# Optimization experiments

Measured on AMD Instinct MI355X. Metric: run time of the kernel, lower is better.

Reference implementation:

```python
import jax, jax.numpy as jnp
import numpy as np
import math

B, T, D = 8, 1024, 1024
N, L = 256, 768
H = 16
TE = 2048  # time_embed_dim
EPS = 1e-5


def _ln(x, g, b):
    mu = jnp.mean(x, axis=-1, keepdims=True)
    var = jnp.mean(jnp.square(x - mu), axis=-1, keepdims=True)
    return (x - mu) * jax.lax.rsqrt(var + EPS) * g + b


def setup_inputs() -> dict:
    key = jax.random.key(0)
    ks = jax.random.split(key, 16)
    s = lambda fan_in: 1.0 / math.sqrt(fan_in)
    return {
        "x": jax.random.normal(ks[0], (B, T, D), jnp.float32),
        "xf": jax.random.normal(ks[1], (B, N, L), jnp.float32),
        "emb": jax.random.normal(ks[2], (B, TE), jnp.float32),
        "ln_g": jnp.ones((D,), jnp.float32),
        "ln_b": jnp.zeros((D,), jnp.float32),
        "cln_g": jnp.ones((L,), jnp.float32),
        "cln_b": jnp.zeros((L,), jnp.float32),
        "Wq": jax.random.normal(ks[3], (D, D), jnp.float32) * s(D),
        "bq": jnp.zeros((D,), jnp.float32),
        "Wk": jax.random.normal(ks[4], (L, D), jnp.float32) * s(L),
        "bk": jnp.zeros((D,), jnp.float32),
        "Wv": jax.random.normal(ks[5], (L, D), jnp.float32) * s(L),
        "bv": jnp.zeros((D,), jnp.float32),
        "sln_g": jnp.ones((D,), jnp.float32),
        "sln_b": jnp.zeros((D,), jnp.float32),
        "Wemb": jax.random.normal(ks[6], (TE, 2 * D), jnp.float32) * s(TE),
        "bemb": jnp.zeros((2 * D,), jnp.float32),
        "Wout": jax.random.normal(ks[7], (D, D), jnp.float32) * s(D) * 0.02,
        "bout": jnp.zeros((D,), jnp.float32),
    }


def reference(x, xf, emb, ln_g, ln_b, cln_g, cln_b, Wq, bq, Wk, bk, Wv, bv,
              sln_g, sln_b, Wemb, bemb, Wout, bout):
    # x: (B,T,D), xf: (B,N,L), emb: (B,TE)
    hd = D // H
    q = (_ln(x, ln_g, ln_b) @ Wq + bq).reshape(B, T, H, hd)
    xf_n = _ln(xf, cln_g, cln_b)
    k = (xf_n @ Wk + bk).reshape(B, N, H, hd)
    v = (xf_n @ Wv + bv).reshape(B, N, H, hd)
    # scores: (B,T,N,H); note: scaled by sqrt(D//H)
    att = jnp.einsum('bthd,bnhd->btnh', q, k) / math.sqrt(hd)
    w = jax.nn.softmax(att, axis=2)  # softmax over conditioning tokens N
    y = jnp.einsum('btnh,bnhd->bthd', w, v).reshape(B, T, D)
    # StylizationBlock (dropout = 0)
    emb_out = jax.nn.silu(emb) @ Wemb + bemb  # (B, 2D)
    scale, shift = jnp.split(emb_out[:, None, :], 2, axis=2)
    h = _ln(y, sln_g, sln_b) * (1.0 + scale) + shift
    h = jax.nn.silu(h) @ Wout + bout
    return x + h
```

## Files before the change

kernel.cpp:

```cpp
#include <hip/hip_runtime.h>
#include <hip/hip_bf16.h>

typedef __hip_bfloat16 bf16;
typedef unsigned short ushort;
typedef __attribute__((ext_vector_type(8))) short bf16x8;
typedef __attribute__((ext_vector_type(4))) float f32x4;

#define B_ 8
#define T_ 1024
#define D_ 1024
#define N_ 256
#define L_ 768
#define H_ 16
#define HD_ 64
#define TE_ 2048

__device__ __forceinline__ void gld16(const void* g, void* l) {
    __builtin_amdgcn_global_load_lds((const __attribute__((address_space(1))) void*)g,
                                     (__attribute__((address_space(3))) void*)l,
                                     16, 0, 0);
}

__device__ __forceinline__ float bitf(unsigned u) { return __uint_as_float(u); }

__global__ __launch_bounds__(256) void prep_kernel(
        const float* __restrict__ x, const float* __restrict__ xf,
        const float* __restrict__ g1, const float* __restrict__ b1,
        const float* __restrict__ g2, const float* __restrict__ b2,
        const float* __restrict__ Wq, const float* __restrict__ Wk,
        const float* __restrict__ Wv, const float* __restrict__ Wo,
        const float* __restrict__ emb, const float* __restrict__ Wemb,
        bf16* __restrict__ out1, bf16* __restrict__ out2,
        bf16* __restrict__ wqt, bf16* __restrict__ wkt,
        bf16* __restrict__ wvt, bf16* __restrict__ wot,
        float* __restrict__ part) {
    __shared__ __align__(16) char smem[16384];
    int bid = blockIdx.x;
    int tid = threadIdx.x;
    if (bid < 10240) {
        const float *rp, *g, *bb; bf16* op; int cols;
        if (bid < B_ * T_) {
            rp = x + (size_t)bid * D_; g = g1; bb = b1; op = out1 + (size_t)bid * D_; cols = D_;
        } else {
            int r = bid - B_ * T_;
            rp = xf + (size_t)r * L_; g = g2; bb = b2; op = out2 + (size_t)r * L_; cols = L_;
        }
        float* ps  = (float*)smem;
        float* ps2 = ps + 4;
        float* st  = ps + 8;
        bool act = tid * 4 < cols;
        float4 v = act ? *(const float4*)&rp[tid * 4] : make_float4(0.f, 0.f, 0.f, 0.f);
        float s = v.x + v.y + v.z + v.w;
        float s2 = v.x * v.x + v.y * v.y + v.z * v.z + v.w * v.w;
        for (int off = 32; off; off >>= 1) {
            s  += __shfl_down(s,  off, 64);
            s2 += __shfl_down(s2, off, 64);
        }
        int wid = tid >> 6, lid = tid & 63;
        if (lid == 0) { ps[wid] = s; ps2[wid] = s2; }
        __syncthreads();
        if (tid == 0) {
            float t = ps[0] + ps[1] + ps[2] + ps[3];
            float t2 = ps2[0] + ps2[1] + ps2[2] + ps2[3];
            float m = t / cols;
            float var = t2 / cols - m * m;
            st[0] = m; st[1] = rsqrtf(var + 1e-5f);
        }
        __syncthreads();
        if (!act) return;
        float mu = st[0], rstd = st[1];
        float4 gv = *(const float4*)&g[tid * 4];
        float4 bv = *(const float4*)&bb[tid * 4];
        float o0 = (v.x - mu) * rstd * gv.x + bv.x;
        float o1 = (v.y - mu) * rstd * gv.y + bv.y;
        float o2 = (v.z - mu) * rstd * gv.z + bv.z;
        float o3 = (v.w - mu) * rstd * gv.w + bv.w;
        ushort4 uo;
        bf16 h0 = __float2bfloat16(o0); uo.x = *(ushort*)&h0;
        bf16 h1 = __float2bfloat16(o1); uo.y = *(ushort*)&h1;
        bf16 h2 = __float2bfloat16(o2); uo.z = *(ushort*)&h2;
        bf16 h3 = __float2bfloat16(o3); uo.w = *(ushort*)&h3;
        *(ushort4*)&op[tid * 4] = uo;
    } else if (bid < 11136) {
        ushort (*t)[65] = (ushort(*)[65])smem;
        int id = bid - 10240;
        int xb = id & 15, y = id >> 4;
        const float* W; bf16* Wt; int K, ky;
        if (y < 16)      { W = Wq; Wt = wqt; K = 1024; ky = y; }
        else if (y < 28) { W = Wk; Wt = wkt; K = 768;  ky = y - 16; }
        else if (y < 40) { W = Wv; Wt = wvt; K = 768;  ky = y - 28; }
        else             { W = Wo; Wt = wot; K = 1024; ky = y - 40; }
        int k0 = ky * 64, n0 = xb * 64;
#pragma unroll
        for (int i = 0; i < 16; i++) {
            int e = tid + i * 256;
            int r = e >> 6, c = e & 63;
            bf16 hv = __float2bfloat16(W[(size_t)(k0 + r) * D_ + n0 + c]);
            t[r][c] = *(ushort*)&hv;
        }
        __syncthreads();
#pragma unroll
        for (int i = 0; i < 16; i++) {
            int e = tid + i * 256;
            int r = e >> 6, c = e & 63;
            ushort uv = t[c][r];
            Wt[(size_t)(n0 + r) * K + k0 + c] = *(bf16*)&uv;
        }
    } else {
        float* se  = (float*)smem;
        float* red = (float*)(smem + 8192);
        int id = bid - 11136;
        int j0 = (id & 31) * 64;
        int ks = id >> 5;
        int tx = tid & 15, ty = tid >> 4;
        int w = tid >> 6, lane = tid & 63;
#pragma unroll
        for (int b = 0; b < 8; b++) {
            float xv = emb[b * TE_ + ks * 256 + tid];
            se[b * 256 + tid] = xv / (1.f + __expf(-xv));
        }
        __syncthreads();
        float acc[8][4] = {};
#pragma unroll 4
        for (int i = 0; i < 16; i++) {
            int e = ty + 16 * i;
            float4 wv = *(const float4*)&Wemb[(size_t)(ks * 256 + e) * 2048 + j0 + tx * 4];
#pragma unroll
            for (int b = 0; b < 8; b++) {
                float s = se[b * 256 + e];
                acc[b][0] += s * wv.x; acc[b][1] += s * wv.y;
                acc[b][2] += s * wv.z; acc[b][3] += s * wv.w;
            }
        }
#pragma unroll
        for (int b = 0; b < 8; b++)
#pragma unroll
            for (int m = 0; m < 4; m++) {
                float v = acc[b][m];
                v += __shfl_down(v, 32, 64);
                v += __shfl_down(v, 16, 64);
                if (lane < 16) red[(w * 8 + b) * 64 + lane * 4 + m] = v;
            }
        __syncthreads();
        for (int o = tid; o < 512; o += 256) {
            int b = o >> 6, jl = o & 63;
            float s = red[(0 * 8 + b) * 64 + jl] + red[(1 * 8 + b) * 64 + jl]
                    + red[(2 * 8 + b) * 64 + jl] + red[(3 * 8 + b) * 64 + jl];
            part[((size_t)ks * 8 + b) * 2048 + j0 + jl] = s;
        }
    }
}

template <int MODE>
__device__ __forceinline__ void gemm_body(const ushort* __restrict__ Ap,
                                          const ushort* __restrict__ Bp,
                                          const float* __restrict__ bias,
                                          const float* __restrict__ res,
                                          void* __restrict__ Cout,
                                          int m0, int n0, int Ncols, int K,
                                          ushort* Ash, ushort* Bsh) {
    int tid = threadIdx.x;
    int w = tid >> 6, lane = tid & 63;
    int quad = lane >> 4, l15 = lane & 15;
    int wm = (w >> 1) * 64, wn = (w & 1) * 32;
    int lr8 = lane >> 3;
    int sc  = lane & 7;
    int gc  = sc ^ lr8;
    f32x4 acc[4][2] = {};
    for (int kt = 0; kt < K; kt += 64) {
#pragma unroll
        for (int j = 0; j < 4; j++) {
            int rbase = w * 32 + j * 8;
            gld16(&Ap[(size_t)(m0 + rbase + lr8) * K + kt + gc * 8], &Ash[rbase * 64]);
        }
#pragma unroll
        for (int j = 0; j < 2; j++) {
            int rbase = w * 16 + j * 8;
            gld16(&Bp[(size_t)(n0 + rbase + lr8) * K + kt + gc * 8], &Bsh[rbase * 64]);
        }
        __syncthreads();
#pragma unroll
        for (int kh = 0; kh < 2; kh++) {
            bf16x8 af[4], bfr[2];
#pragma unroll
            for (int mt = 0; mt < 4; mt++)
                af[mt] = *(bf16x8*)&Ash[(wm + mt * 16 + l15) * 64 + (((kh * 4 + quad) ^ (l15 & 7)) * 8)];
#pragma unroll
            for (int nt = 0; nt < 2; nt++)
                bfr[nt] = *(bf16x8*)&Bsh[(wn + nt * 16 + l15) * 64 + (((kh * 4 + quad) ^ (l15 & 7)) * 8)];
#pragma unroll
            for (int mt = 0; mt < 4; mt++)
#pragma unroll
                for (int nt = 0; nt < 2; nt++)
                    acc[mt][nt] = __builtin_amdgcn_mfma_f32_16x16x32_bf16(af[mt], bfr[nt], acc[mt][nt], 0, 0, 0);
        }
        __syncthreads();
    }
#pragma unroll
    for (int mt = 0; mt < 4; mt++) {
#pragma unroll
        for (int nt = 0; nt < 2; nt++) {
#pragma unroll
            for (int reg = 0; reg < 4; reg++) {
                int row = m0 + wm + mt * 16 + quad * 4 + reg;
                int col = n0 + wn + nt * 16 + l15;
                float v = acc[mt][nt][reg] + bias[col];
                if (MODE == 1) {
                    v += res[(size_t)row * Ncols + col];
                    ((float*)Cout)[(size_t)row * Ncols + col] = v;
                } else if (MODE == 0) {
                    ((bf16*)Cout)[(size_t)row * Ncols + col] = __float2bfloat16(v);
                } else {
                    int b = row >> 8, n = row & 255;
                    int h = col >> 6, d = col & 63;
                    size_t addr = ((size_t)(b * 16 + h) * 64 + d) * 256
                                + (((n >> 3) ^ (d & 7)) * 8) + (n & 7);
                    ((bf16*)Cout)[addr] = __float2bfloat16(v);
                }
            }
        }
    }
}

__global__ __launch_bounds__(256) void qkv_gemm(const bf16* __restrict__ xn,
                                                const bf16* __restrict__ xfn,
                                                const bf16* __restrict__ wqt,
                                                const bf16* __restrict__ wkt,
                                                const bf16* __restrict__ wvt,
                                                const float* __restrict__ bq,
                                                const float* __restrict__ bk,
                                                const float* __restrict__ bv,
                                                bf16* __restrict__ q,
                                                bf16* __restrict__ kbuf,
                                                bf16* __restrict__ vT,
                                                const float* __restrict__ part,
                                                const float* __restrict__ bemb,
                                                float* __restrict__ embo) {
    __shared__ ushort Ash[128 * 64];
    __shared__ ushort Bsh[64 * 64];
    int bid = blockIdx.x;
    if (bid < 1024) {
        gemm_body<0>((const ushort*)xn, (const ushort*)wqt, bq, nullptr, q,
                     (bid & 63) * 128, (bid >> 6) * 64, D_, D_, Ash, Bsh);
    } else if (bid < 1280) {
        int id = bid - 1024;
        gemm_body<0>((const ushort*)xfn, (const ushort*)wkt, bk, nullptr, kbuf,
                     (id & 15) * 128, (id >> 4) * 64, D_, L_, Ash, Bsh);
    } else if (bid < 1536) {
        int id = bid - 1280;
        gemm_body<2>((const ushort*)xfn, (const ushort*)wvt, bv, nullptr, vT,
                     (id & 15) * 128, (id >> 4) * 64, D_, L_, Ash, Bsh);
    } else {
        int o = (bid - 1536) * 256 + threadIdx.x;
        int b = o >> 11, j = o & 2047;
        float s = bemb[j];
#pragma unroll
        for (int ks = 0; ks < 8; ks++) s += part[((size_t)ks * 8 + b) * 2048 + j];
        embo[o] = s;
    }
}

__global__ __launch_bounds__(256) void out_gemm(const bf16* __restrict__ a,
                                                const bf16* __restrict__ wot,
                                                const float* __restrict__ bout,
                                                const float* __restrict__ x,
                                                float* __restrict__ out) {
    __shared__ ushort Ash[128 * 64];
    __shared__ ushort Bsh[64 * 64];
    int bid = blockIdx.x;
    gemm_body<1>((const ushort*)a, (const ushort*)wot, bout, x, out,
                 (bid & 63) * 128, (bid >> 6) * 64, D_, D_, Ash, Bsh);
}

__global__ __launch_bounds__(256) void attn_mfma(const bf16* __restrict__ q,
                                                 const bf16* __restrict__ k,
                                                 const bf16* __restrict__ vT,
                                                 bf16* __restrict__ y) {
    __shared__ ushort KV[N_ * HD_];
    __shared__ ushort P[64 * N_];
    int tid = threadIdx.x;
    int w = tid >> 6, lane = tid & 63;
    int quad = lane >> 4, l15 = lane & 15;
    int t0 = blockIdx.x * 64;
    int bh = blockIdx.y;
    int b = bh >> 4, h = bh & 15;

    const ushort* kp = (const ushort*)k;
    const ushort* qp = (const ushort*)q;
    const ushort* vp = (const ushort*)vT;
    int lr8 = lane >> 3, sc = lane & 7, gc = sc ^ lr8;

#pragma unroll
    for (int j = 0; j < 8; j++) {
        int rbase = w * 64 + j * 8;
        gld16(&kp[(size_t)(b * N_ + rbase + lr8) * D_ + h * 64 + gc * 8], &KV[rbase * 64]);
    }
#pragma unroll
    for (int j = 0; j < 2; j++) {
        int rbase = w * 16 + j * 8;
        gld16(&qp[(size_t)(b * T_ + t0 + rbase + lr8) * D_ + h * 64 + gc * 8], &P[rbase * 64]);
    }
    __syncthreads();

    int qrow = w * 16 + l15;
    bf16x8 aq[2];
#pragma unroll
    for (int kk = 0; kk < 2; kk++)
        aq[kk] = *(bf16x8*)&P[qrow * 64 + (((kk * 4 + quad) ^ (qrow & 7)) * 8)];
    f32x4 sf[16];
#pragma unroll
    for (int nt = 0; nt < 16; nt++) {
        int n = nt * 16 + l15;
        bf16x8 b0 = *(bf16x8*)&KV[n * 64 + (((0 + quad) ^ (n & 7)) * 8)];
        bf16x8 b1 = *(bf16x8*)&KV[n * 64 + (((4 + quad) ^ (n & 7)) * 8)];
        f32x4 z = {};
        f32x4 t = __builtin_amdgcn_mfma_f32_16x16x32_bf16(aq[0], b0, z, 0, 0, 0);
        sf[nt] = __builtin_amdgcn_mfma_f32_16x16x32_bf16(aq[1], b1, t, 0, 0, 0);
    }
    __syncthreads();

    const ushort* vbase = vp + (size_t)(b * 16 + h) * 16384;
#pragma unroll
    for (int j = 0; j < 8; j++) {
        gld16(&vbase[(w * 8 + j) * 512 + lane * 8], &KV[(w * 8 + j) * 512]);
    }

    const float scale = 0.125f;
    float mx[4] = {-1e30f, -1e30f, -1e30f, -1e30f};
#pragma unroll
    for (int nt = 0; nt < 16; nt++)
#pragma unroll
        for (int reg = 0; reg < 4; reg++) mx[reg] = fmaxf(mx[reg], sf[nt][reg]);
#pragma unroll
    for (int off = 1; off < 16; off <<= 1)
#pragma unroll
        for (int reg = 0; reg < 4; reg++)
            mx[reg] = fmaxf(mx[reg], __shfl_xor(mx[reg], off, 64));
    float sm[4] = {0.f, 0.f, 0.f, 0.f};
#pragma unroll
    for (int nt = 0; nt < 16; nt++)
#pragma unroll
        for (int reg = 0; reg < 4; reg++) {
            float e = __expf((sf[nt][reg] - mx[reg]) * scale);
            sf[nt][reg] = e;
            sm[reg] += e;
        }
#pragma unroll
    for (int off = 1; off < 16; off <<= 1)
#pragma unroll
        for (int reg = 0; reg < 4; reg++)
            sm[reg] += __shfl_xor(sm[reg], off, 64);
    float inv[4];
#pragma unroll
    for (int reg = 0; reg < 4; reg++) inv[reg] = 1.f / sm[reg];

#pragma unroll
    for (int nt = 0; nt < 16; nt++)
#pragma unroll
        for (int reg = 0; reg < 4; reg++) {
            int r = w * 16 + quad * 4 + reg;
            int colc = nt * 2 + (l15 >> 3);
            int addr = r * 256 + ((colc ^ (r & 7)) * 8) + (l15 & 7);
            bf16 hv = __float2bfloat16(sf[nt][reg]);
            P[addr] = *(ushort*)&hv;
        }
    __syncthreads();

    f32x4 of[4] = {};
    int prow = w * 16 + l15;
#pragma unroll
    for (int kk = 0; kk < 8; kk++) {
        bf16x8 ap = *(bf16x8*)&P[prow * 256 + (((kk * 4 + quad) ^ (prow & 7)) * 8)];
#pragma unroll
        for (int dt = 0; dt < 4; dt++) {
            int d = dt * 16 + l15;
            bf16x8 bv = *(bf16x8*)&KV[d * 256 + (((kk * 4 + quad) ^ (d & 7)) * 8)];
            of[dt] = __builtin_amdgcn_mfma_f32_16x16x32_bf16(ap, bv, of[dt], 0, 0, 0);
        }
    }
#pragma unroll
    for (int dt = 0; dt < 4; dt++)
#pragma unroll
        for (int reg = 0; reg < 4; reg++) {
            int r = t0 + w * 16 + quad * 4 + reg;
            y[((size_t)(b * T_ + r) * D_) + h * 64 + dt * 16 + l15] =
                __float2bfloat16(of[dt][reg] * inv[reg]);
        }
}

__global__ __launch_bounds__(256) void styl_kernel(const bf16* __restrict__ y,
                                                   const float* __restrict__ g,
                                                   const float* __restrict__ bb,
                                                   const float* __restrict__ embo,
                                                   bf16* __restrict__ a) {
    int row = blockIdx.x;
    int b = row >> 10;
    int tid = threadIdx.x;
    const ushort* rp = (const ushort*)(y + (size_t)row * D_);
    ushort4 uy = *(const ushort4*)&rp[tid * 4];
    float v0 = bitf((unsigned)uy.x << 16), v1 = bitf((unsigned)uy.y << 16);
    float v2 = bitf((unsigned)uy.z << 16), v3 = bitf((unsigned)uy.w << 16);
    float s = v0 + v1 + v2 + v3;
    float s2 = v0 * v0 + v1 * v1 + v2 * v2 + v3 * v3;
    for (int off = 32; off; off >>= 1) {
        s  += __shfl_down(s,  off, 64);
        s2 += __shfl_down(s2, off, 64);
    }
    __shared__ float ps[4], ps2[4];
    __shared__ float smu, srstd;
    int wid = tid >> 6, lid = tid & 63;
    if (lid == 0) { ps[wid] = s; ps2[wid] = s2; }
    __syncthreads();
    if (tid == 0) {
        float t = ps[0] + ps[1] + ps[2] + ps[3];
        float t2 = ps2[0] + ps2[1] + ps2[2] + ps2[3];
        float m = t / D_;
        float var = t2 / D_ - m * m;
        smu = m; srstd = rsqrtf(var + 1e-5f);
    }
    __syncthreads();
    float mu = smu, rstd = srstd;
    float4 gv = *(const float4*)&g[tid * 4];
    float4 bv = *(const float4*)&bb[tid * 4];
    float4 scv = *(const float4*)&embo[b * 2048 + tid * 4];
    float4 shv = *(const float4*)&embo[b * 2048 + 1024 + tid * 4];
    float n0 = (v0 - mu) * rstd * gv.x + bv.x;
    float n1 = (v1 - mu) * rstd * gv.y + bv.y;
    float n2 = (v2 - mu) * rstd * gv.z + bv.z;
    float n3 = (v3 - mu) * rstd * gv.w + bv.w;
    float h0 = n0 * (1.f + scv.x) + shv.x;
    float h1 = n1 * (1.f + scv.y) + shv.y;
    float h2 = n2 * (1.f + scv.z) + shv.z;
    float h3 = n3 * (1.f + scv.w) + shv.w;
    h0 = h0 / (1.f + __expf(-h0));
    h1 = h1 / (1.f + __expf(-h1));
    h2 = h2 / (1.f + __expf(-h2));
    h3 = h3 / (1.f + __expf(-h3));
    ushort4 uo;
    bf16 t0 = __float2bfloat16(h0); uo.x = *(ushort*)&t0;
    bf16 t1 = __float2bfloat16(h1); uo.y = *(ushort*)&t1;
    bf16 t2 = __float2bfloat16(h2); uo.z = *(ushort*)&t2;
    bf16 t3 = __float2bfloat16(h3); uo.w = *(ushort*)&t3;
    *(ushort4*)&((ushort*)a)[(size_t)row * D_ + tid * 4] = uo;
}

extern "C" void kernel_launch(void* const* d_in, const int* in_sizes, int n_in,
                              void* d_out, int out_size, void* d_ws, size_t ws_size,
                              hipStream_t stream) {
    const float* x    = (const float*)d_in[0];
    const float* xf   = (const float*)d_in[1];
    const float* emb  = (const float*)d_in[2];
    const float* ln_g = (const float*)d_in[3];
    const float* ln_b = (const float*)d_in[4];
    const float* cln_g= (const float*)d_in[5];
    const float* cln_b= (const float*)d_in[6];
    const float* Wq   = (const float*)d_in[7];
    const float* bq   = (const float*)d_in[8];
    const float* Wk   = (const float*)d_in[9];
    const float* bk   = (const float*)d_in[10];
    const float* Wv   = (const float*)d_in[11];
    const float* bv   = (const float*)d_in[12];
    const float* sln_g= (const float*)d_in[13];
    const float* sln_b= (const float*)d_in[14];
    const float* Wemb = (const float*)d_in[15];
    const float* bemb = (const float*)d_in[16];
    const float* Wout = (const float*)d_in[17];
    const float* bout = (const float*)d_in[18];
    float* out = (float*)d_out;

    char* wsp = (char*)d_ws;
    bf16*  xn   = (bf16*)(wsp);
    bf16*  xfn  = (bf16*)(wsp + 16777216);
    bf16*  q    = (bf16*)(wsp + 19922944);
    bf16*  kbuf = (bf16*)(wsp + 36700160);
    bf16*  vT   = (bf16*)(wsp + 40894464);
    float* embo = (float*)(wsp + 45088768);
    bf16*  wqt  = (bf16*)(wsp + 45154304);
    bf16*  wkt  = (bf16*)(wsp + 47251456);
    bf16*  wvt  = (bf16*)(wsp + 48824320);
    bf16*  wot  = (bf16*)(wsp + 50397184);
    float* part = (float*)(wsp + 52494336);
    bf16*  ybuf = xn;
    bf16*  abuf = q;

    prep_kernel<<<11392, 256, 0, stream>>>(x, xf, ln_g, ln_b, cln_g, cln_b,
                                           Wq, Wk, Wv, Wout, emb, Wemb,
                                           xn, xfn, wqt, wkt, wvt, wot, part);

    qkv_gemm<<<1600, 256, 0, stream>>>(xn, xfn, wqt, wkt, wvt, bq, bk, bv,
                                       q, kbuf, vT, part, bemb, embo);

    attn_mfma<<<dim3(16, 128), 256, 0, stream>>>(q, kbuf, vT, ybuf);

    styl_kernel<<<B_ * T_, 256, 0, stream>>>(ybuf, sln_g, sln_b, embo, abuf);

    out_gemm<<<1024, 256, 0, stream>>>(abuf, wot, bout, x, out);
}
```

Baseline: 255.8 us.

## Switch projection GEMMs from bf16 to fp8 MFMA operands

Normalized activations, transposed weights and the stylized activation are now quantized to fp8 instead of bf16, and both the QKV and output GEMMs use the fp8 16x16x32 MFMA with 128-wide K tiles. This halves operand bytes written and read and halves the K-loop trip count. The LDS layout and swizzle change to suit 8-byte fragments. It risks accuracy loss from fp8 rounding of activations and weights, and the workspace layout is reorganized.

```diff
diff --git a/kernel.cpp b/kernel.cpp
--- a/kernel.cpp
+++ b/kernel.cpp
@@ -3,6 +3,8 @@
 
 typedef __hip_bfloat16 bf16;
 typedef unsigned short ushort;
+typedef unsigned char uchar;
+typedef long i64;
 typedef __attribute__((ext_vector_type(8))) short bf16x8;
 typedef __attribute__((ext_vector_type(4))) float f32x4;
 
@@ -23,6 +25,16 @@
 
 __device__ __forceinline__ float bitf(unsigned u) { return __uint_as_float(u); }
 
+__device__ __forceinline__ int pk4_fp8(float a, float b, float c, float d) {
+    int p = __builtin_amdgcn_cvt_pk_fp8_f32(a, b, 0, false);
+    p = __builtin_amdgcn_cvt_pk_fp8_f32(c, d, p, true);
+    return p;
+}
+__device__ __forceinline__ uchar pk1_fp8(float a) {
+    int p = __builtin_amdgcn_cvt_pk_fp8_f32(a, a, 0, false);
+    return (uchar)(p & 0xff);
+}
+
 __global__ __launch_bounds__(256) void prep_kernel(
         const float* __restrict__ x, const float* __restrict__ xf,
         const float* __restrict__ g1, const float* __restrict__ b1,
@@ -30,20 +42,20 @@
         const float* __restrict__ Wq, const float* __restrict__ Wk,
         const float* __restrict__ Wv, const float* __restrict__ Wo,
         const float* __restrict__ emb, const float* __restrict__ Wemb,
-        bf16* __restrict__ out1, bf16* __restrict__ out2,
-        bf16* __restrict__ wqt, bf16* __restrict__ wkt,
-        bf16* __restrict__ wvt, bf16* __restrict__ wot,
+        uchar* __restrict__ xn8, uchar* __restrict__ xfn8,
+        uchar* __restrict__ wq8, uchar* __restrict__ wk8,
+        uchar* __restrict__ wv8, uchar* __restrict__ wo8,
         float* __restrict__ part) {
     __shared__ __align__(16) char smem[16384];
     int bid = blockIdx.x;
     int tid = threadIdx.x;
     if (bid < 10240) {
-        const float *rp, *g, *bb; bf16* op; int cols;
+        const float *rp, *g, *bb; uchar* op; int cols;
         if (bid < B_ * T_) {
-            rp = x + (size_t)bid * D_; g = g1; bb = b1; op = out1 + (size_t)bid * D_; cols = D_;
+            rp = x + (size_t)bid * D_; g = g1; bb = b1; op = xn8 + (size_t)bid * D_; cols = D_;
         } else {
             int r = bid - B_ * T_;
-            rp = xf + (size_t)r * L_; g = g2; bb = b2; op = out2 + (size_t)r * L_; cols = L_;
+            rp = xf + (size_t)r * L_; g = g2; bb = b2; op = xfn8 + (size_t)r * L_; cols = L_;
         }
         float* ps  = (float*)smem;
         float* ps2 = ps + 4;
@@ -75,36 +87,31 @@
         float o1 = (v.y - mu) * rstd * gv.y + bv.y;
         float o2 = (v.z - mu) * rstd * gv.z + bv.z;
         float o3 = (v.w - mu) * rstd * gv.w + bv.w;
-        ushort4 uo;
-        bf16 h0 = __float2bfloat16(o0); uo.x = *(ushort*)&h0;
-        bf16 h1 = __float2bfloat16(o1); uo.y = *(ushort*)&h1;
-        bf16 h2 = __float2bfloat16(o2); uo.z = *(ushort*)&h2;
-        bf16 h3 = __float2bfloat16(o3); uo.w = *(ushort*)&h3;
-        *(ushort4*)&op[tid * 4] = uo;
+        *(int*)&op[tid * 4] = pk4_fp8(o0, o1, o2, o3);
     } else if (bid < 11136) {
-        ushort (*t)[65] = (ushort(*)[65])smem;
+        uchar (*t)[65] = (uchar(*)[65])smem;
         int id = bid - 10240;
         int xb = id & 15, y = id >> 4;
-        const float* W; bf16* Wt; int K, ky;
-        if (y < 16)      { W = Wq; Wt = wqt; K = 1024; ky = y; }
-        else if (y < 28) { W = Wk; Wt = wkt; K = 768;  ky = y - 16; }
-        else if (y < 40) { W = Wv; Wt = wvt; K = 768;  ky = y - 28; }
-        else             { W = Wo; Wt = wot; K = 1024; ky = y - 40; }
+        const float* W; uchar* Wt; int K, ky;
+        if (y < 16)      { W = Wq; Wt = wq8; K = 1024; ky = y; }
+        else if (y < 28) { W = Wk; Wt = wk8; K = 768;  ky = y - 16; }
+        else if (y < 40) { W = Wv; Wt = wv8; K = 768;  ky = y - 28; }
+        else             { W = Wo; Wt = wo8; K = 1024; ky = y - 40; }
         int k0 = ky * 64, n0 = xb * 64;
 #pragma unroll
         for (int i = 0; i < 16; i++) {
             int e = tid + i * 256;
             int r = e >> 6, c = e & 63;
-            bf16 hv = __float2bfloat16(W[(size_t)(k0 + r) * D_ + n0 + c]);
-            t[r][c] = *(ushort*)&hv;
-        }
-        __syncthreads();
-#pragma unroll
-        for (int i = 0; i < 16; i++) {
+            t[r][c] = pk1_fp8(W[(size_t)(k0 + r) * D_ + n0 + c]);
+        }
+        __syncthreads();
+#pragma unroll
+        for (int i = 0; i < 4; i++) {
             int e = tid + i * 256;
-            int r = e >> 6, c = e & 63;
-            ushort uv = t[c][r];
-            Wt[(size_t)(n0 + r) * K + k0 + c] = *(bf16*)&uv;
+            int r = e >> 4, cg = (e & 15) * 4;
+            unsigned u = (unsigned)t[cg][r] | ((unsigned)t[cg + 1][r] << 8)
+                       | ((unsigned)t[cg + 2][r] << 16) | ((unsigned)t[cg + 3][r] << 24);
+            *(unsigned*)&Wt[(size_t)(n0 + r) * K + k0 + cg] = u;
         }
     } else {
         float* se  = (float*)smem;
@@ -152,13 +159,13 @@
 }
 
 template <int MODE>
-__device__ __forceinline__ void gemm_body(const ushort* __restrict__ Ap,
-                                          const ushort* __restrict__ Bp,
+__device__ __forceinline__ void gemm_body(const uchar* __restrict__ Ap,
+                                          const uchar* __restrict__ Bp,
                                           const float* __restrict__ bias,
                                           const float* __restrict__ res,
                                           void* __restrict__ Cout,
                                           int m0, int n0, int Ncols, int K,
-                                          ushort* Ash, ushort* Bsh) {
+                                          uchar* Ash, uchar* Bsh) {
     int tid = threadIdx.x;
     int w = tid >> 6, lane = tid & 63;
     int quad = lane >> 4, l15 = lane & 15;
@@ -167,32 +174,35 @@
     int sc  = lane & 7;
     int gc  = sc ^ lr8;
     f32x4 acc[4][2] = {};
-    for (int kt = 0; kt < K; kt += 64) {
+    for (int kt = 0; kt < K; kt += 128) {
 #pragma unroll
         for (int j = 0; j < 4; j++) {
             int rbase = w * 32 + j * 8;
-            gld16(&Ap[(size_t)(m0 + rbase + lr8) * K + kt + gc * 8], &Ash[rbase * 64]);
+            gld16(&Ap[(size_t)(m0 + rbase + lr8) * K + kt + gc * 16], &Ash[rbase * 128]);
         }
 #pragma unroll
         for (int j = 0; j < 2; j++) {
             int rbase = w * 16 + j * 8;
-            gld16(&Bp[(size_t)(n0 + rbase + lr8) * K + kt + gc * 8], &Bsh[rbase * 64]);
-        }
-        __syncthreads();
-#pragma unroll
-        for (int kh = 0; kh < 2; kh++) {
-            bf16x8 af[4], bfr[2];
+            gld16(&Bp[(size_t)(n0 + rbase + lr8) * K + kt + gc * 16], &Bsh[rbase * 128]);
+        }
+        __syncthreads();
+#pragma unroll
+        for (int kh = 0; kh < 4; kh++) {
+            int c4 = kh * 2 + (quad >> 1);
+            int sub = (quad & 1) * 8;
+            int pos = (c4 ^ (l15 & 7)) * 16 + sub;
+            i64 af[4], bfr[2];
 #pragma unroll
             for (int mt = 0; mt < 4; mt++)
-                af[mt] = *(bf16x8*)&Ash[(wm + mt * 16 + l15) * 64 + (((kh * 4 + quad) ^ (l15 & 7)) * 8)];
+                af[mt] = *(const i64*)&Ash[(wm + mt * 16 + l15) * 128 + pos];
 #pragma unroll
             for (int nt = 0; nt < 2; nt++)
-                bfr[nt] = *(bf16x8*)&Bsh[(wn + nt * 16 + l15) * 64 + (((kh * 4 + quad) ^ (l15 & 7)) * 8)];
+                bfr[nt] = *(const i64*)&Bsh[(wn + nt * 16 + l15) * 128 + pos];
 #pragma unroll
             for (int mt = 0; mt < 4; mt++)
 #pragma unroll
                 for (int nt = 0; nt < 2; nt++)
-                    acc[mt][nt] = __builtin_amdgcn_mfma_f32_16x16x32_bf16(af[mt], bfr[nt], acc[mt][nt], 0, 0, 0);
+                    acc[mt][nt] = __builtin_amdgcn_mfma_f32_16x16x32_fp8_fp8(af[mt], bfr[nt], acc[mt][nt], 0, 0, 0);
         }
         __syncthreads();
     }
@@ -222,11 +232,11 @@
     }
 }
 
-__global__ __launch_bounds__(256) void qkv_gemm(const bf16* __restrict__ xn,
-                                                const bf16* __restrict__ xfn,
-                                                const bf16* __restrict__ wqt,
-                                                const bf16* __restrict__ wkt,
-                                                const bf16* __restrict__ wvt,
+__global__ __launch_bounds__(256) void qkv_gemm(const uchar* __restrict__ xn8,
+                                                const uchar* __restrict__ xfn8,
+                                                const uchar* __restrict__ wq8,
+                                                const uchar* __restrict__ wk8,
+                                                const uchar* __restrict__ wv8,
                                                 const float* __restrict__ bq,
                                                 const float* __restrict__ bk,
                                                 const float* __restrict__ bv,
@@ -236,19 +246,19 @@
                                                 const float* __restrict__ part,
                                                 const float* __restrict__ bemb,
                                                 float* __restrict__ embo) {
-    __shared__ ushort Ash[128 * 64];
-    __shared__ ushort Bsh[64 * 64];
+    __shared__ __align__(16) uchar Ash[128 * 128];
+    __shared__ __align__(16) uchar Bsh[64 * 128];
     int bid = blockIdx.x;
     if (bid < 1024) {
-        gemm_body<0>((const ushort*)xn, (const ushort*)wqt, bq, nullptr, q,
+        gemm_body<0>(xn8, wq8, bq, nullptr, q,
                      (bid & 63) * 128, (bid >> 6) * 64, D_, D_, Ash, Bsh);
     } else if (bid < 1280) {
         int id = bid - 1024;
-        gemm_body<0>((const ushort*)xfn, (const ushort*)wkt, bk, nullptr, kbuf,
+        gemm_body<0>(xfn8, wk8, bk, nullptr, kbuf,
                      (id & 15) * 128, (id >> 4) * 64, D_, L_, Ash, Bsh);
     } else if (bid < 1536) {
         int id = bid - 1280;
-        gemm_body<2>((const ushort*)xfn, (const ushort*)wvt, bv, nullptr, vT,
+        gemm_body<2>(xfn8, wv8, bv, nullptr, vT,
                      (id & 15) * 128, (id >> 4) * 64, D_, L_, Ash, Bsh);
     } else {
         int o = (bid - 1536) * 256 + threadIdx.x;
@@ -260,15 +270,15 @@
     }
 }
 
-__global__ __launch_bounds__(256) void out_gemm(const bf16* __restrict__ a,
-                                                const bf16* __restrict__ wot,
+__global__ __launch_bounds__(256) void out_gemm(const uchar* __restrict__ a8,
+                                                const uchar* __restrict__ wo8,
                                                 const float* __restrict__ bout,
                                                 const float* __restrict__ x,
                                                 float* __restrict__ out) {
-    __shared__ ushort Ash[128 * 64];
-    __shared__ ushort Bsh[64 * 64];
+    __shared__ __align__(16) uchar Ash[128 * 128];
+    __shared__ __align__(16) uchar Bsh[64 * 128];
     int bid = blockIdx.x;
-    gemm_body<1>((const ushort*)a, (const ushort*)wot, bout, x, out,
+    gemm_body<1>(a8, wo8, bout, x, out,
                  (bid & 63) * 128, (bid >> 6) * 64, D_, D_, Ash, Bsh);
 }
 
@@ -392,7 +402,7 @@
                                                    const float* __restrict__ g,
                                                    const float* __restrict__ bb,
                                                    const float* __restrict__ embo,
-                                                   bf16* __restrict__ a) {
+                                                   uchar* __restrict__ a8) {
     int row = blockIdx.x;
     int b = row >> 10;
     int tid = threadIdx.x;
@@ -436,12 +446,7 @@
     h1 = h1 / (1.f + __expf(-h1));
     h2 = h2 / (1.f + __expf(-h2));
     h3 = h3 / (1.f + __expf(-h3));
-    ushort4 uo;
-    bf16 t0 = __float2bfloat16(h0); uo.x = *(ushort*)&t0;
-    bf16 t1 = __float2bfloat16(h1); uo.y = *(ushort*)&t1;
-    bf16 t2 = __float2bfloat16(h2); uo.z = *(ushort*)&t2;
-    bf16 t3 = __float2bfloat16(h3); uo.w = *(ushort*)&t3;
-    *(ushort4*)&((ushort*)a)[(size_t)row * D_ + tid * 4] = uo;
+    *(int*)&a8[(size_t)row * D_ + tid * 4] = pk4_fp8(h0, h1, h2, h3);
 }
 
 extern "C" void kernel_launch(void* const* d_in, const int* in_sizes, int n_in,
@@ -469,30 +474,31 @@
     float* out = (float*)d_out;
 
     char* wsp = (char*)d_ws;
-    bf16*  xn   = (bf16*)(wsp);
-    bf16*  xfn  = (bf16*)(wsp + 16777216);
-    bf16*  q    = (bf16*)(wsp + 19922944);
-    bf16*  kbuf = (bf16*)(wsp + 36700160);
-    bf16*  vT   = (bf16*)(wsp + 40894464);
-    float* embo = (float*)(wsp + 45088768);
-    bf16*  wqt  = (bf16*)(wsp + 45154304);
-    bf16*  wkt  = (bf16*)(wsp + 47251456);
-    bf16*  wvt  = (bf16*)(wsp + 48824320);
-    bf16*  wot  = (bf16*)(wsp + 50397184);
-    float* part = (float*)(wsp + 52494336);
-    bf16*  ybuf = xn;
-    bf16*  abuf = q;
+    const size_t MB = 1024 * 1024;
+    uchar* xn8  = (uchar*)(wsp);
+    uchar* xfn8 = (uchar*)(wsp + 8 * MB);
+    uchar* wq8  = (uchar*)(wsp + 10 * MB);
+    uchar* wk8  = (uchar*)(wsp + 11 * MB);
+    uchar* wv8  = (uchar*)(wsp + 12 * MB);
+    uchar* wo8  = (uchar*)(wsp + 13 * MB);
+    bf16*  q    = (bf16*)(wsp + 14 * MB);
+    bf16*  kbuf = (bf16*)(wsp + 30 * MB);
+    bf16*  vT   = (bf16*)(wsp + 34 * MB);
+    bf16*  ybuf = (bf16*)(wsp + 38 * MB);
+    uchar* a8   = (uchar*)(wsp + 54 * MB);
+    float* embo = (float*)(wsp + 62 * MB);
+    float* part = (float*)(wsp + 63 * MB);
 
     prep_kernel<<<11392, 256, 0, stream>>>(x, xf, ln_g, ln_b, cln_g, cln_b,
                                            Wq, Wk, Wv, Wout, emb, Wemb,
-                                           xn, xfn, wqt, wkt, wvt, wot, part);
-
-    qkv_gemm<<<1600, 256, 0, stream>>>(xn, xfn, wqt, wkt, wvt, bq, bk, bv,
+                                           xn8, xfn8, wq8, wk8, wv8, wo8, part);
+
+    qkv_gemm<<<1600, 256, 0, stream>>>(xn8, xfn8, wq8, wk8, wv8, bq, bk, bv,
                                        q, kbuf, vT, part, bemb, embo);
 
     attn_mfma<<<dim3(16, 128), 256, 0, stream>>>(q, kbuf, vT, ybuf);
 
-    styl_kernel<<<B_ * T_, 256, 0, stream>>>(ybuf, sln_g, sln_b, embo, abuf);
-
-    out_gemm<<<1024, 256, 0, stream>>>(abuf, wot, bout, x, out);
-}
+    styl_kernel<<<B_ * T_, 256, 0, stream>>>(ybuf, sln_g, sln_b, embo, a8);
+
+    out_gemm<<<1024, 256, 0, stream>>>(a8, wo8, bout, x, out);
+}
```

Result: faster. 242.0 us (-5.4%).
